# Kernel tuning notes

Measured on AMD Instinct MI355X. Metric: run time of the kernel, lower is better.

The kernel has to match this reference:

```python
import jax, jax.numpy as jnp
import numpy as np

N_NODES = 100000
N_EDGES = 1000000
D = 64            # node_hidden
IN_DIM = 4 * D    # 256
MLP_H = 32
EPS = 1e-5


def setup_inputs() -> dict:
    key = jax.random.key(0)
    ks = jax.random.split(key, 6)
    h = jax.random.normal(ks[0], (N_NODES, D), dtype=jnp.float32)
    edge_pairs = jax.random.randint(ks[1], (2, N_EDGES), 0, N_NODES, dtype=jnp.int64)
    # LayerNorm params
    gamma = jnp.ones((IN_DIM,), dtype=jnp.float32)
    beta = jnp.zeros((IN_DIM,), dtype=jnp.float32)
    # MLP params (PyTorch Linear default init: U(-1/sqrt(fan_in), 1/sqrt(fan_in)))
    b1_bound = 1.0 / np.sqrt(IN_DIM)
    W1 = jax.random.uniform(ks[2], (IN_DIM, MLP_H), minval=-b1_bound, maxval=b1_bound, dtype=jnp.float32)
    b1 = jax.random.uniform(ks[3], (MLP_H,), minval=-b1_bound, maxval=b1_bound, dtype=jnp.float32)
    b2_bound = 1.0 / np.sqrt(MLP_H)
    W2 = jax.random.uniform(ks[4], (MLP_H, 1), minval=-b2_bound, maxval=b2_bound, dtype=jnp.float32)
    b2 = jax.random.uniform(ks[5], (1,), minval=-b2_bound, maxval=b2_bound, dtype=jnp.float32)
    return {"h": h, "edge_pairs": edge_pairs, "gamma": gamma, "beta": beta,
            "W1": W1, "b1": b1, "W2": W2, "b2": b2}


def reference(h, edge_pairs, gamma, beta, W1, b1, W2, b2):
    u = h[edge_pairs[0]]                                    # [E, D]
    v = h[edge_pairs[1]]                                    # [E, D]
    feat = jnp.concatenate([u, v, jnp.abs(u - v), u * v], axis=-1)  # [E, 4D]
    mu = jnp.mean(feat, axis=-1, keepdims=True)
    var = jnp.mean(jnp.square(feat - mu), axis=-1, keepdims=True)
    feat = (feat - mu) * jax.lax.rsqrt(var + EPS) * gamma + beta
    hmid = jax.nn.relu(feat @ W1 + b1)                      # [E, MLP_H]; dropout inactive at eval
    logit = hmid @ W2 + b2                                  # [E, 1]
    return logit.reshape(-1)
```

## Files before the change

kernel.cpp:

```cpp
#include <hip/hip_runtime.h>
#include <hip/hip_bf16.h>

#define N_EDGES 1000000
#define N_TILES (N_EDGES / 16)
#define N_NODES 100000

typedef __attribute__((ext_vector_type(8))) short short8;
typedef __attribute__((ext_vector_type(4))) float floatx4;

__device__ __forceinline__ short f2bf(float f) {
    __bf16 b = (__bf16)f;
    return __builtin_bit_cast(short, b);
}

union BU { short8 s8; __hip_bfloat162 b2[4]; };
__device__ __forceinline__ void dp8(short8 a, short8 b, short8& d, short8& p) {
    BU ua, ub, ud, up;
    ua.s8 = a; ub.s8 = b;
#pragma unroll
    for (int i = 0; i < 4; ++i) {
        ud.b2[i] = __hsub2(ua.b2[i], ub.b2[i]);
        up.b2[i] = __hmul2(ua.b2[i], ub.b2[i]);
    }
#pragma unroll
    for (int j = 0; j < 8; ++j) ud.s8[j] = (short)(ud.s8[j] & 0x7fff);
    d = ud.s8; p = up.s8;
}

__global__ __launch_bounds__(256) void conv_kernel(const float* __restrict__ h,
                                                   unsigned short* __restrict__ hb) {
    const int i = blockIdx.x * blockDim.x + threadIdx.x;
    if (i >= (N_NODES * 64) / 8) return;
    const float* p = h + (long)i * 8;
    floatx4 a = *(const floatx4*)p;
    floatx4 b = *(const floatx4*)(p + 4);
    short8 o;
    o[0] = f2bf(a[0]); o[1] = f2bf(a[1]); o[2] = f2bf(a[2]); o[3] = f2bf(a[3]);
    o[4] = f2bf(b[0]); o[5] = f2bf(b[1]); o[6] = f2bf(b[2]); o[7] = f2bf(b[3]);
    *(short8*)(hb + (long)i * 8) = o;
}

__global__ __launch_bounds__(256) void wprep_kernel(const float* __restrict__ gamma,
                                                    const float* __restrict__ beta,
                                                    const float* __restrict__ W1,
                                                    unsigned short* __restrict__ Wt,
                                                    float* __restrict__ GB) {
    const int n = blockIdx.x;
    const int k = threadIdx.x;
    const float w1 = W1[k * 32 + n];
    float G = gamma[k] * w1;
    float B = beta[k] * w1;
    Wt[n * 256 + k] = (unsigned short)f2bf(G);
    G += __shfl_xor(G, 1);  B += __shfl_xor(B, 1);
    G += __shfl_xor(G, 2);  B += __shfl_xor(B, 2);
    G += __shfl_xor(G, 4);  B += __shfl_xor(B, 4);
    G += __shfl_xor(G, 8);  B += __shfl_xor(B, 8);
    G += __shfl_xor(G, 16); B += __shfl_xor(B, 16);
    G += __shfl_xor(G, 32); B += __shfl_xor(B, 32);
    __shared__ float sG[4], sB[4];
    if ((k & 63) == 0) { sG[k >> 6] = G; sB[k >> 6] = B; }
    __syncthreads();
    if (k == 0) {
        GB[n]      = sG[0] + sG[1] + sG[2] + sG[3];
        GB[32 + n] = sB[0] + sB[1] + sB[2] + sB[3];
    }
}

__global__ __launch_bounds__(256) void edgehead_kernel(
    const unsigned short* __restrict__ hb,
    const int* __restrict__ ep,
    const float* __restrict__ b1,
    const float* __restrict__ W2,
    const float* __restrict__ b2p,
    const unsigned short* __restrict__ Wt,
    const float* __restrict__ GB,
    float* __restrict__ out)
{
    const int lane = threadIdx.x & 63;
    const int c = lane & 15;
    const int q = lane >> 4;
    const int wid = (int)((blockIdx.x * blockDim.x + threadIdx.x) >> 6);
    const int nw = (int)((gridDim.x * blockDim.x) >> 6);

    __shared__ short lds_wt[32 * 33 * 8];
    for (int idx = threadIdx.x; idx < 1024; idx += 256) {
        const int r = idx >> 5, j = idx & 31;
        *(short8*)(lds_wt + (r * 33 + j) * 8) = *(const short8*)(Wt + r * 256 + 8 * j);
    }
    __syncthreads();

    int wt_off = (c * 33 + q) * 8;
    short8 ones;
#pragma unroll
    for (int j = 0; j < 8; ++j) ones[j] = (short)0x3F80;

    short8 wsel;
#pragma unroll
    for (int j = 0; j < 8; ++j) wsel[j] = (c == 4 * q + (j & 3)) ? (short)0x3F80 : (short)0;

    const float Gn0 = GB[c],      Gn1 = GB[16 + c];
    const float Bn0 = GB[32 + c] + b1[c];
    const float Bn1 = GB[48 + c] + b1[16 + c];
    const float W20 = W2[c],      W21 = W2[16 + c];
    const float b2  = b2p[0];

    int t = wid;
    if (t >= N_TILES) return;

    int s0 = ep[t * 16 + c];
    int d0 = ep[N_EDGES + t * 16 + c];
    short8 au0 = *(const short8*)(hb + (long)s0 * 64 + 8 * q);
    short8 au1 = *(const short8*)(hb + (long)s0 * 64 + 8 * q + 32);
    short8 av0 = *(const short8*)(hb + (long)d0 * 64 + 8 * q);
    short8 av1 = *(const short8*)(hb + (long)d0 * 64 + 8 * q + 32);
    int t1 = t + nw;
    int e1 = (t1 < N_TILES ? t1 : t) * 16 + c;
    int s1i = ep[e1];
    int d1i = ep[N_EDGES + e1];

    for (; t < N_TILES; t += nw) {
        asm("" : "+v"(wt_off));

        short8 nu0 = *(const short8*)(hb + (long)s1i * 64 + 8 * q);
        short8 nu1 = *(const short8*)(hb + (long)s1i * 64 + 8 * q + 32);
        short8 nv0 = *(const short8*)(hb + (long)d1i * 64 + 8 * q);
        short8 nv1 = *(const short8*)(hb + (long)d1i * 64 + 8 * q + 32);
        {
            const int tn = t + 2 * nw;
            const int en = (tn < N_TILES ? tn : t) * 16 + c;
            s1i = ep[en];
            d1i = ep[N_EDGES + en];
        }

        short8 ad0, ad1, ap0, ap1;
        dp8(au0, av0, ad0, ap0);
        dp8(au1, av1, ad1, ap1);

        floatx4 acc0 = {0.f, 0.f, 0.f, 0.f};
        floatx4 acc1 = {0.f, 0.f, 0.f, 0.f};
        floatx4 asum = {0.f, 0.f, 0.f, 0.f};
        floatx4 agrm = {0.f, 0.f, 0.f, 0.f};
#pragma unroll
        for (int s = 0; s < 8; ++s) {
            short8 af;
            switch (s) {
                case 0: af = au0; break;
                case 1: af = au1; break;
                case 2: af = av0; break;
                case 3: af = av1; break;
                case 4: af = ad0; break;
                case 5: af = ad1; break;
                case 6: af = ap0; break;
                default: af = ap1; break;
            }
            const short8 bf0 = *(const short8*)(lds_wt + wt_off + s * 32);
            const short8 bf1 = *(const short8*)(lds_wt + wt_off + 16 * 33 * 8 + s * 32);
            acc0 = __builtin_amdgcn_mfma_f32_16x16x32_bf16(af, bf0,  acc0, 0, 0, 0);
            acc1 = __builtin_amdgcn_mfma_f32_16x16x32_bf16(af, bf1,  acc1, 0, 0, 0);
            asum = __builtin_amdgcn_mfma_f32_16x16x32_bf16(af, ones, asum, 0, 0, 0);
            agrm = __builtin_amdgcn_mfma_f32_16x16x32_bf16(af, af,   agrm, 0, 0, 0);
        }

        float ss[4];
#pragma unroll
        for (int r = 0; r < 4; ++r) ss[r] = __shfl(agrm[r], 20 * q + r);
        short8 af2;
#pragma unroll
        for (int r = 0; r < 4; ++r) {
            const float mu  = asum[r] * (1.f / 256.f);
            const float var = fmaf(ss[r], 1.f / 256.f, -mu * mu);
            const float rs  = rsqrtf(var + 1e-5f);
            float h0 = fmaf(rs, fmaf(-mu, Gn0, acc0[r]), Bn0); h0 = fmaxf(h0, 0.f);
            float h1 = fmaf(rs, fmaf(-mu, Gn1, acc1[r]), Bn1); h1 = fmaxf(h1, 0.f);
            af2[r]     = f2bf(h0 * W20);
            af2[4 + r] = f2bf(h1 * W21);
        }
        floatx4 dfin = {0.f, 0.f, 0.f, 0.f};
        dfin = __builtin_amdgcn_mfma_f32_16x16x32_bf16(af2, wsel, dfin, 0, 0, 0);
        float part = (dfin[0] + dfin[1]) + (dfin[2] + dfin[3]);
        part += __shfl_xor(part, 16);
        part += __shfl_xor(part, 32);
        if (q == 0) out[t * 16 + c] = part + b2;

        au0 = nu0; au1 = nu1; av0 = nv0; av1 = nv1;
    }
}

extern "C" void kernel_launch(void* const* d_in, const int* in_sizes, int n_in,
                              void* d_out, int out_size, void* d_ws, size_t ws_size,
                              hipStream_t stream) {
    const float* h     = (const float*)d_in[0];
    const int*   ep    = (const int*)d_in[1];
    const float* gamma = (const float*)d_in[2];
    const float* beta  = (const float*)d_in[3];
    const float* W1    = (const float*)d_in[4];
    const float* b1    = (const float*)d_in[5];
    const float* W2    = (const float*)d_in[6];
    const float* b2    = (const float*)d_in[7];
    float* out = (float*)d_out;

    unsigned short* hb = (unsigned short*)d_ws;
    unsigned short* Wt = (unsigned short*)((char*)d_ws + 12800000);
    float* GB = (float*)((char*)d_ws + 12800000 + 16384);

    conv_kernel<<<(N_NODES * 64 / 8 + 255) / 256, 256, 0, stream>>>(h, hb);
    wprep_kernel<<<32, 256, 0, stream>>>(gamma, beta, W1, Wt, GB);
    edgehead_kernel<<<2048, 256, 0, stream>>>(hb, ep, b1, W2, b2, Wt, GB, out);
}
```

Baseline: 132.0 us.

## Deepen gather prefetch pipeline to triple-buffered rows with indices five tiles ahead

Restructures the edge loop into a three-way unrolled rotation so row gathers are issued two tiles ahead and edge indices five tiles ahead, where before they were one and two tiles ahead. This is meant to hide more of the random-access gather latency behind MFMA work. It also recomputes |u-v| and u*v inline within the MFMA loop, which shortens their live ranges. In exchange it holds more registers for the extra buffered rows, which may lower occupancy.

```diff
diff --git a/kernel.cpp b/kernel.cpp
--- a/kernel.cpp
+++ b/kernel.cpp
@@ -6,6 +6,7 @@
 #define N_NODES 100000
 
 typedef __attribute__((ext_vector_type(8))) short short8;
+typedef __attribute__((ext_vector_type(4))) int intx4;
 typedef __attribute__((ext_vector_type(4))) float floatx4;
 
 __device__ __forceinline__ short f2bf(float f) {
@@ -13,18 +14,22 @@
     return __builtin_bit_cast(short, b);
 }
 
-union BU { short8 s8; __hip_bfloat162 b2[4]; };
-__device__ __forceinline__ void dp8(short8 a, short8 b, short8& d, short8& p) {
-    BU ua, ub, ud, up;
+union BI { short8 s8; intx4 i4; __hip_bfloat162 b2[4]; };
+
+__device__ __forceinline__ short8 dabs8(short8 a, short8 b) {
+    BI ua, ub, ud;
     ua.s8 = a; ub.s8 = b;
 #pragma unroll
-    for (int i = 0; i < 4; ++i) {
-        ud.b2[i] = __hsub2(ua.b2[i], ub.b2[i]);
-        up.b2[i] = __hmul2(ua.b2[i], ub.b2[i]);
-    }
-#pragma unroll
-    for (int j = 0; j < 8; ++j) ud.s8[j] = (short)(ud.s8[j] & 0x7fff);
-    d = ud.s8; p = up.s8;
+    for (int i = 0; i < 4; ++i) ud.b2[i] = __hsub2(ua.b2[i], ub.b2[i]);
+    ud.i4 &= 0x7fff7fff;
+    return ud.s8;
+}
+__device__ __forceinline__ short8 pmul8(short8 a, short8 b) {
+    BI ua, ub, up;
+    ua.s8 = a; ub.s8 = b;
+#pragma unroll
+    for (int i = 0; i < 4; ++i) up.b2[i] = __hmul2(ua.b2[i], ub.b2[i]);
+    return up.s8;
 }
 
 __global__ __launch_bounds__(256) void conv_kernel(const float* __restrict__ h,
@@ -107,83 +112,91 @@
     int t = wid;
     if (t >= N_TILES) return;
 
-    int s0 = ep[t * 16 + c];
-    int d0 = ep[N_EDGES + t * 16 + c];
-    short8 au0 = *(const short8*)(hb + (long)s0 * 64 + 8 * q);
-    short8 au1 = *(const short8*)(hb + (long)s0 * 64 + 8 * q + 32);
-    short8 av0 = *(const short8*)(hb + (long)d0 * 64 + 8 * q);
-    short8 av1 = *(const short8*)(hb + (long)d0 * 64 + 8 * q + 32);
-    int t1 = t + nw;
-    int e1 = (t1 < N_TILES ? t1 : t) * 16 + c;
-    int s1i = ep[e1];
-    int d1i = ep[N_EDGES + e1];
-
-    for (; t < N_TILES; t += nw) {
-        asm("" : "+v"(wt_off));
-
-        short8 nu0 = *(const short8*)(hb + (long)s1i * 64 + 8 * q);
-        short8 nu1 = *(const short8*)(hb + (long)s1i * 64 + 8 * q + 32);
-        short8 nv0 = *(const short8*)(hb + (long)d1i * 64 + 8 * q);
-        short8 nv1 = *(const short8*)(hb + (long)d1i * 64 + 8 * q + 32);
-        {
-            const int tn = t + 2 * nw;
-            const int en = (tn < N_TILES ? tn : t) * 16 + c;
-            s1i = ep[en];
-            d1i = ep[N_EDGES + en];
-        }
-
-        short8 ad0, ad1, ap0, ap1;
-        dp8(au0, av0, ad0, ap0);
-        dp8(au1, av1, ad1, ap1);
-
-        floatx4 acc0 = {0.f, 0.f, 0.f, 0.f};
-        floatx4 acc1 = {0.f, 0.f, 0.f, 0.f};
-        floatx4 asum = {0.f, 0.f, 0.f, 0.f};
-        floatx4 agrm = {0.f, 0.f, 0.f, 0.f};
-#pragma unroll
-        for (int s = 0; s < 8; ++s) {
-            short8 af;
-            switch (s) {
-                case 0: af = au0; break;
-                case 1: af = au1; break;
-                case 2: af = av0; break;
-                case 3: af = av1; break;
-                case 4: af = ad0; break;
-                case 5: af = ad1; break;
-                case 6: af = ap0; break;
-                default: af = ap1; break;
-            }
-            const short8 bf0 = *(const short8*)(lds_wt + wt_off + s * 32);
-            const short8 bf1 = *(const short8*)(lds_wt + wt_off + 16 * 33 * 8 + s * 32);
-            acc0 = __builtin_amdgcn_mfma_f32_16x16x32_bf16(af, bf0,  acc0, 0, 0, 0);
-            acc1 = __builtin_amdgcn_mfma_f32_16x16x32_bf16(af, bf1,  acc1, 0, 0, 0);
-            asum = __builtin_amdgcn_mfma_f32_16x16x32_bf16(af, ones, asum, 0, 0, 0);
-            agrm = __builtin_amdgcn_mfma_f32_16x16x32_bf16(af, af,   agrm, 0, 0, 0);
-        }
-
-        float ss[4];
-#pragma unroll
-        for (int r = 0; r < 4; ++r) ss[r] = __shfl(agrm[r], 20 * q + r);
-        short8 af2;
-#pragma unroll
-        for (int r = 0; r < 4; ++r) {
-            const float mu  = asum[r] * (1.f / 256.f);
-            const float var = fmaf(ss[r], 1.f / 256.f, -mu * mu);
-            const float rs  = rsqrtf(var + 1e-5f);
-            float h0 = fmaf(rs, fmaf(-mu, Gn0, acc0[r]), Bn0); h0 = fmaxf(h0, 0.f);
-            float h1 = fmaf(rs, fmaf(-mu, Gn1, acc1[r]), Bn1); h1 = fmaxf(h1, 0.f);
-            af2[r]     = f2bf(h0 * W20);
-            af2[4 + r] = f2bf(h1 * W21);
-        }
-        floatx4 dfin = {0.f, 0.f, 0.f, 0.f};
-        dfin = __builtin_amdgcn_mfma_f32_16x16x32_bf16(af2, wsel, dfin, 0, 0, 0);
-        float part = (dfin[0] + dfin[1]) + (dfin[2] + dfin[3]);
-        part += __shfl_xor(part, 16);
-        part += __shfl_xor(part, 32);
-        if (q == 0) out[t * 16 + c] = part + b2;
-
-        au0 = nu0; au1 = nu1; av0 = nv0; av1 = nv1;
+#define IDX_LOAD(tt, S, D) { int _t = (tt); if (_t >= N_TILES) _t = wid;          \
+                             const int _e = _t * 16 + c;                          \
+                             S = ep[_e]; D = ep[N_EDGES + _e]; }
+#define ROW_ISSUE(S, D, U0, U1, V0, V1)                                           \
+    U0 = *(const short8*)(hb + (long)(S) * 64 + 8 * q);                           \
+    U1 = *(const short8*)(hb + (long)(S) * 64 + 8 * q + 32);                      \
+    V0 = *(const short8*)(hb + (long)(D) * 64 + 8 * q);                           \
+    V1 = *(const short8*)(hb + (long)(D) * 64 + 8 * q + 32);
+
+    short8 aU0, aU1, aV0, aV1;
+    short8 bU0, bU1, bV0, bV1;
+    short8 cU0, cU1, cV0, cV1;
+    int sA, dA, sB, dB, sC, dC;
+
+    IDX_LOAD(t,          sA, dA);
+    IDX_LOAD(t + nw,     sB, dB);
+    IDX_LOAD(t + 2 * nw, sC, dC);
+    ROW_ISSUE(sA, dA, aU0, aU1, aV0, aV1);
+    ROW_ISSUE(sB, dB, bU0, bU1, bV0, bV1);
+    IDX_LOAD(t + 3 * nw, sA, dA);
+    IDX_LOAD(t + 4 * nw, sB, dB);
+
+#define BODY(U0, U1, V0, V1, NU0, NU1, NV0, NV1, SN, DN)                          \
+  {                                                                               \
+    if (t >= N_TILES) goto tail;                                                  \
+    asm("" : "+v"(wt_off));        \
+    ROW_ISSUE(SN, DN, NU0, NU1, NV0, NV1);                                        \
+    IDX_LOAD(t + 5 * nw, SN, DN);                                                 \
+    floatx4 acc0 = {0.f, 0.f, 0.f, 0.f};                                          \
+    floatx4 acc1 = {0.f, 0.f, 0.f, 0.f};                                          \
+    floatx4 asum = {0.f, 0.f, 0.f, 0.f};                            \
+    floatx4 agrm = {0.f, 0.f, 0.f, 0.f};         \
+    _Pragma("unroll")                                                             \
+    for (int s = 0; s < 8; ++s) {                                                 \
+      short8 af;                                                                  \
+      switch (s) {                                                                \
+        case 0: af = U0; break;                                                   \
+        case 1: af = U1; break;                                                   \
+        case 2: af = V0; break;                                                   \
+        case 3: af = V1; break;                                                   \
+        case 4: af = dabs8(U0, V0); break;           \
+        case 5: af = dabs8(U1, V1); break;                                        \
+        case 6: af = pmul8(U0, V0); break;                                        \
+        default: af = pmul8(U1, V1); break;                                       \
+      }                                                                           \
+      const short8 bf0 = *(const short8*)(lds_wt + wt_off + s * 32);              \
+      const short8 bf1 = *(const short8*)(lds_wt + wt_off + 16 * 33 * 8 + s * 32);\
+      acc0 = __builtin_amdgcn_mfma_f32_16x16x32_bf16(af, bf0,  acc0, 0, 0, 0);    \
+      acc1 = __builtin_amdgcn_mfma_f32_16x16x32_bf16(af, bf1,  acc1, 0, 0, 0);    \
+      asum = __builtin_amdgcn_mfma_f32_16x16x32_bf16(af, ones, asum, 0, 0, 0);    \
+      agrm = __builtin_amdgcn_mfma_f32_16x16x32_bf16(af, af,   agrm, 0, 0, 0);    \
+    }                                                                             \
+    float ss[4];                                                                  \
+    _Pragma("unroll")                                                             \
+    for (int r = 0; r < 4; ++r) ss[r] = __shfl(agrm[r], 20 * q + r);              \
+    short8 af2;                                                                   \
+    _Pragma("unroll")                                                             \
+    for (int r = 0; r < 4; ++r) {                                                 \
+      const float mu  = asum[r] * (1.f / 256.f);                                  \
+      const float var = fmaf(ss[r], 1.f / 256.f, -mu * mu);                       \
+      const float rs  = rsqrtf(var + 1e-5f);                                      \
+      float h0 = fmaf(rs, fmaf(-mu, Gn0, acc0[r]), Bn0); h0 = fmaxf(h0, 0.f);     \
+      float h1 = fmaf(rs, fmaf(-mu, Gn1, acc1[r]), Bn1); h1 = fmaxf(h1, 0.f);     \
+      af2[r]     = f2bf(h0 * W20);                                                \
+      af2[4 + r] = f2bf(h1 * W21);                                                \
+    }                                                                             \
+    floatx4 dfin = {0.f, 0.f, 0.f, 0.f};                                          \
+    dfin = __builtin_amdgcn_mfma_f32_16x16x32_bf16(af2, wsel, dfin, 0, 0, 0);     \
+    float part = (dfin[0] + dfin[1]) + (dfin[2] + dfin[3]);                       \
+    part += __shfl_xor(part, 16);                                                 \
+    part += __shfl_xor(part, 32);                                                 \
+    if (q == 0) out[t * 16 + c] = part + b2;             \
+    t += nw;                                                                      \
+  }
+
+    for (;;) {
+        BODY(aU0, aU1, aV0, aV1, cU0, cU1, cV0, cV1, sC, dC);
+        BODY(bU0, bU1, bV0, bV1, aU0, aU1, aV0, aV1, sA, dA);
+        BODY(cU0, cU1, cV0, cV1, bU0, bU1, bV0, bV1, sB, dB);
     }
+tail:
+    return;
+#undef BODY
+#undef ROW_ISSUE
+#undef IDX_LOAD
 }
 
 extern "C" void kernel_launch(void* const* d_in, const int* in_sizes, int n_in,
```

New measurement: 134.0 us. About the same (+1.6%).
